# Performance work log

Measured on AMD Instinct MI355X. Metric: run time of the kernel, lower is better.

Reference implementation:

```python
import jax, jax.numpy as jnp
import numpy as np

EMBED = 64
HEADS = 8
N, S = 8, 1024


def setup_inputs() -> dict:
    key = jax.random.key(0)
    ks = jax.random.split(key, 8)
    scale = 1.0 / np.sqrt(EMBED)
    return {
        "values": jax.random.normal(ks[0], (N, S, EMBED), dtype=jnp.float32),
        "keys": jax.random.normal(ks[1], (N, S, EMBED), dtype=jnp.float32),
        "queries": jax.random.normal(ks[2], (N, S, EMBED), dtype=jnp.float32),
        # per-head projection weights, torch Linear convention: y = x @ W.T
        "Wv": jax.random.normal(ks[3], (HEADS, EMBED, EMBED), dtype=jnp.float32) * scale,
        "Wk": jax.random.normal(ks[4], (HEADS, EMBED, EMBED), dtype=jnp.float32) * scale,
        "Wq": jax.random.normal(ks[5], (HEADS, EMBED, EMBED), dtype=jnp.float32) * scale,
        "Wout": jax.random.normal(ks[6], (EMBED, HEADS * EMBED), dtype=jnp.float32) * (1.0 / np.sqrt(HEADS * EMBED)),
        "bout": jnp.zeros((EMBED,), dtype=jnp.float32),
    }


def reference(values, keys, queries, Wv, Wk, Wq, Wout, bout):
    d = queries.shape[-1]
    # Batched per-head projections (each head keeps full embed dim, per the module)
    v = jnp.einsum("nkd,hed->nhke", values, Wv)   # [N,H,K,D]
    k = jnp.einsum("nkd,hed->nhke", keys, Wk)     # [N,H,K,D]
    q = jnp.einsum("nqd,hed->nhqe", queries, Wq)  # [N,H,Q,D]
    energy = jnp.einsum("nhqd,nhkd->nhqk", q, k)
    attn = jax.nn.softmax(energy / jnp.sqrt(jnp.asarray(d, energy.dtype)), axis=-1)  # [N,H,Q,K]
    head_out = jnp.einsum("nhqk,nhkd->nhqd", attn, v)  # [N,H,Q,D]
    # torch.cat(output_heads, dim=2) == transpose heads next to feature then flatten
    nN, nH, nQ, nD = head_out.shape
    cat = jnp.transpose(head_out, (0, 2, 1, 3)).reshape(nN, nQ, nH * nD)  # [N,Q,H*D]
    out = cat @ Wout.T + bout  # [N,Q,D]
    return out, attn
```

## Files before the change

kernel.cpp:

```cpp
#include <hip/hip_runtime.h>

typedef __bf16 bf16x8 __attribute__((ext_vector_type(8)));
typedef float  f32x4  __attribute__((ext_vector_type(4)));

#define MFMA16(a, b, c) __builtin_amdgcn_mfma_f32_16x16x32_bf16((a), (b), (c), 0, 0, 0)

constexpr int N_ = 8, H_ = 8, S_ = 1024, D_ = 64;

__global__ __launch_bounds__(256) void proj_kernel(
    const float* __restrict__ Xq, const float* __restrict__ Xk,
    const float* __restrict__ Xv,
    const float* __restrict__ Wq, const float* __restrict__ Wk,
    const float* __restrict__ Wv,
    unsigned short* __restrict__ qb_, unsigned short* __restrict__ kb_,
    unsigned short* __restrict__ vtb_)
{
    __shared__ __bf16 T[64 * 72];

    const int which = blockIdx.y;
    const float* X = (which == 0) ? Xq : (which == 1) ? Xk : Xv;
    const float* W = (which == 0) ? Wq : (which == 1) ? Wk : Wv;

    const int b   = blockIdx.x;
    const int st  = b & 15;
    const int h   = (b >> 4) & 7;
    const int n   = b >> 7;
    const int s0  = st * 64;
    const int nh  = n * H_ + h;
    const int tid = threadIdx.x;
    const int w = tid >> 6, lane = tid & 63;
    const int l16 = lane & 15, quad = lane >> 4;

    const float* xrow = X + (size_t)(n * S_ + s0 + w * 16 + l16) * D_;
    bf16x8 a[2];
#pragma unroll
    for (int half = 0; half < 2; ++half) {
        const float* p = xrow + half * 32 + quad * 8;
        f32x4 x0 = *(const f32x4*)p;
        f32x4 x1 = *(const f32x4*)(p + 4);
#pragma unroll
        for (int j = 0; j < 4; ++j) { a[half][j] = (__bf16)x0[j]; a[half][4 + j] = (__bf16)x1[j]; }
    }

#pragma unroll
    for (int et = 0; et < 4; ++et) {
        const int e0 = et * 16;
        f32x4 acc = {0.f, 0.f, 0.f, 0.f};
#pragma unroll
        for (int half = 0; half < 2; ++half) {
            const float* wp = W + ((size_t)(h * 64 + e0 + l16)) * 64 + half * 32 + quad * 8;
            f32x4 x0 = *(const f32x4*)wp;
            f32x4 x1 = *(const f32x4*)(wp + 4);
            bf16x8 bf;
#pragma unroll
            for (int j = 0; j < 4; ++j) { bf[j] = (__bf16)x0[j]; bf[4 + j] = (__bf16)x1[j]; }
            acc = MFMA16(a[half], bf, acc);
        }
#pragma unroll
        for (int r = 0; r < 4; ++r) {
            const int sl = w * 16 + quad * 4 + r;
            const int e  = e0 + l16;
            const __bf16 v = (__bf16)acc[r];
            if (which == 2) T[e * 72 + sl] = v;
            else            T[sl * 72 + e] = v;
        }
    }
    __syncthreads();

    const int row = tid >> 2, seg = tid & 3;
    const bf16x8 d0 = *(const bf16x8*)&T[row * 72 + seg * 16];
    const bf16x8 d1 = *(const bf16x8*)&T[row * 72 + seg * 16 + 8];
    __bf16* dst;
    if (which == 2)
        dst = (__bf16*)vtb_ + ((size_t)nh * 64 + row) * S_ + s0 + seg * 16;
    else
        dst = (__bf16*)(which == 0 ? qb_ : kb_) + ((size_t)nh * S_ + s0 + row) * D_ + seg * 16;
    *(bf16x8*)dst = d0;
    *(bf16x8*)(dst + 8) = d1;
}

__global__ __launch_bounds__(256, 4) void attn_kernel(
    const unsigned short* __restrict__ qb_, const unsigned short* __restrict__ kb_,
    const unsigned short* __restrict__ vtb_,
    float* __restrict__ attn_out, unsigned short* __restrict__ catb_)
{
    __shared__ __bf16 P[4 * 2 * 16 * 40];

    const __bf16* qb  = (const __bf16*)qb_;
    const __bf16* kb  = (const __bf16*)kb_;
    const __bf16* vtb = (const __bf16*)vtb_;
    __bf16* catb = (__bf16*)catb_;

    const int b  = blockIdx.x;
    const int qt = b & 15;
    const int h  = (b >> 4) & 7;
    const int n  = b >> 7;
    const int nh = n * H_ + h;
    const int q0 = qt * 64;

    const int tid = threadIdx.x;
    const int w = tid >> 6, lane = tid & 63;
    const int l16 = lane & 15, quad = lane >> 4;
    const int m0 = w * 16;

    const __bf16* qbase = qb + ((size_t)nh * S_ + q0 + m0 + l16) * D_;
    const bf16x8 aq0 = *(const bf16x8*)(qbase + quad * 8);
    const bf16x8 aq1 = *(const bf16x8*)(qbase + 32 + quad * 8);

    const __bf16* kbase = kb + ((size_t)nh * S_ + l16) * D_ + quad * 8;

    f32x4 s4 = {0.f, 0.f, 0.f, 0.f};
#pragma unroll 2
    for (int kt = 0; kt < 64; ++kt) {
        const __bf16* kp = kbase + (size_t)kt * 16 * D_;
        const bf16x8 b0 = *(const bf16x8*)kp;
        const bf16x8 b1 = *(const bf16x8*)(kp + 32);
        f32x4 c = {0.f, 0.f, 0.f, 0.f};
        c = MFMA16(aq0, b0, c);
        c = MFMA16(aq1, b1, c);
#pragma unroll
        for (int r = 0; r < 4; ++r) s4[r] += __expf(c[r] * 0.125f);
    }
#pragma unroll
    for (int off = 1; off < 16; off <<= 1) {
#pragma unroll
        for (int r = 0; r < 4; ++r) s4[r] += __shfl_xor(s4[r], off);
    }
    float inv[4];
#pragma unroll
    for (int r = 0; r < 4; ++r) inv[r] = 1.0f / s4[r];

    float* abase = attn_out + ((size_t)nh * S_ + q0 + m0 + quad * 4) * S_ + l16;
    __bf16* Pw = P + w * (2 * 16 * 40);
    const __bf16* vb = vtb + ((size_t)nh * 64 + l16) * S_ + quad * 8;

    f32x4 acc[4] = {{0.f,0.f,0.f,0.f},{0.f,0.f,0.f,0.f},{0.f,0.f,0.f,0.f},{0.f,0.f,0.f,0.f}};

    for (int ch = 0; ch < 32; ++ch) {
        __bf16* Pt = Pw + (ch & 1) * (16 * 40);
#pragma unroll
        for (int hf = 0; hf < 2; ++hf) {
            const int kt = ch * 2 + hf;
            const __bf16* kp = kbase + (size_t)kt * 16 * D_;
            const bf16x8 b0 = *(const bf16x8*)kp;
            const bf16x8 b1 = *(const bf16x8*)(kp + 32);
            f32x4 c = {0.f, 0.f, 0.f, 0.f};
            c = MFMA16(aq0, b0, c);
            c = MFMA16(aq1, b1, c);
#pragma unroll
            for (int r = 0; r < 4; ++r) {
                const float p = __expf(c[r] * 0.125f) * inv[r];
                abase[(size_t)r * S_ + kt * 16] = p;
                Pt[(quad * 4 + r) * 40 + hf * 16 + l16] = (__bf16)p;
            }
        }
        __builtin_amdgcn_sched_barrier(0);
        __builtin_amdgcn_s_waitcnt(0xC07F);
        const bf16x8 af = *(const bf16x8*)&Pt[l16 * 40 + quad * 8];
        __builtin_amdgcn_sched_barrier(0);
#pragma unroll
        for (int et = 0; et < 4; ++et) {
            const bf16x8 bv = *(const bf16x8*)(vb + (size_t)et * 16 * S_ + ch * 32);
            acc[et] = MFMA16(af, bv, acc[et]);
        }
    }

#pragma unroll
    for (int r = 0; r < 4; ++r) {
        const int s = q0 + m0 + quad * 4 + r;
        __bf16* cp = catb + ((size_t)n * S_ + s) * (H_ * D_) + h * D_ + l16;
#pragma unroll
        for (int et = 0; et < 4; ++et) cp[et * 16] = (__bf16)acc[et][r];
    }
}

__global__ __launch_bounds__(256) void outproj_kernel(
    const unsigned short* __restrict__ catb_, const float* __restrict__ Wout,
    const float* __restrict__ bout, float* __restrict__ out)
{
    __shared__ float R[4 * 16 * 68];

    const __bf16* catb = (const __bf16*)catb_;
    const int r0  = blockIdx.x * 16;
    const int tid = threadIdx.x;
    const int w = tid >> 6, lane = tid & 63;
    const int l16 = lane & 15, quad = lane >> 4;
    const int k0 = w * 128;

    const __bf16* arow  = catb + (size_t)(r0 + l16) * 512 + k0 + quad * 8;
    const float*  wbase = Wout + (size_t)l16 * 512 + k0 + quad * 8;

    f32x4 acc[4] = {{0.f,0.f,0.f,0.f},{0.f,0.f,0.f,0.f},{0.f,0.f,0.f,0.f},{0.f,0.f,0.f,0.f}};

#pragma unroll
    for (int kc = 0; kc < 4; ++kc) {
        const bf16x8 af = *(const bf16x8*)(arow + kc * 32);
#pragma unroll
        for (int et = 0; et < 4; ++et) {
            const float* wp = wbase + (size_t)et * 16 * 512 + kc * 32;
            f32x4 x0 = *(const f32x4*)wp;
            f32x4 x1 = *(const f32x4*)(wp + 4);
            bf16x8 bf;
#pragma unroll
            for (int j = 0; j < 4; ++j) { bf[j] = (__bf16)x0[j]; bf[4 + j] = (__bf16)x1[j]; }
            acc[et] = MFMA16(af, bf, acc[et]);
        }
    }
#pragma unroll
    for (int et = 0; et < 4; ++et)
#pragma unroll
        for (int r = 0; r < 4; ++r)
            R[w * (16 * 68) + (quad * 4 + r) * 68 + et * 16 + l16] = acc[et][r];
    __syncthreads();

    const int row = tid >> 4, c0 = (tid & 15) * 4;
    f32x4 s = *(const f32x4*)&R[row * 68 + c0];
#pragma unroll
    for (int wv = 1; wv < 4; ++wv) s += *(const f32x4*)&R[wv * (16 * 68) + row * 68 + c0];
    s += *(const f32x4*)(bout + c0);
    *(f32x4*)(out + (size_t)(r0 + row) * 64 + c0) = s;
}

extern "C" void kernel_launch(void* const* d_in, const int* in_sizes, int n_in,
                              void* d_out, int out_size, void* d_ws, size_t ws_size,
                              hipStream_t stream)
{
    const float* values  = (const float*)d_in[0];
    const float* keys    = (const float*)d_in[1];
    const float* queries = (const float*)d_in[2];
    const float* Wv      = (const float*)d_in[3];
    const float* Wk      = (const float*)d_in[4];
    const float* Wq      = (const float*)d_in[5];
    const float* Wout    = (const float*)d_in[6];
    const float* bout    = (const float*)d_in[7];

    float* out  = (float*)d_out;
    float* attn = out + (size_t)N_ * S_ * D_;

    const size_t nelem = (size_t)N_ * H_ * S_ * D_;
    unsigned short* qb   = (unsigned short*)d_ws;
    unsigned short* kb   = qb  + nelem;
    unsigned short* vtb  = kb  + nelem;
    unsigned short* catb = vtb + nelem;

    proj_kernel<<<dim3(N_ * H_ * (S_ / 64), 3), 256, 0, stream>>>(
        queries, keys, values, Wq, Wk, Wv, qb, kb, vtb);
    attn_kernel<<<N_ * H_ * (S_ / 64), 256, 0, stream>>>(qb, kb, vtb, attn, catb);
    outproj_kernel<<<(N_ * S_) / 16, 256, 0, stream>>>(catb, Wout, bout, out);
}
```

Measured before the change: 479.8 us.

## Split attention key range across waves with 16-query blocks and LDS reduction

Each attention block now handles 16 queries instead of 64. Its four waves split the 1024 keys into quarters rather than splitting the queries. Softmax row sums and the partial PV outputs are combined across waves through shared memory, and the result is written to catb with vectorized bf16x4 stores. The change also quadruples the grid, raises the occupancy hint, and hoists the V loads ahead of the LDS wait. The goal is more parallelism and more coalesced attn writes, at the cost of extra syncthreads and LDS reduction traffic.

New measurement: 561.1 us. 16.9% more time.

```diff
diff --git a/kernel.cpp b/kernel.cpp
--- a/kernel.cpp
+++ b/kernel.cpp
@@ -1,6 +1,7 @@
 #include <hip/hip_runtime.h>
 
 typedef __bf16 bf16x8 __attribute__((ext_vector_type(8)));
+typedef __bf16 bf16x4 __attribute__((ext_vector_type(4)));
 typedef float  f32x4  __attribute__((ext_vector_type(4)));
 
 #define MFMA16(a, b, c) __builtin_amdgcn_mfma_f32_16x16x32_bf16((a), (b), (c), 0, 0, 0)
@@ -79,12 +80,12 @@
     *(bf16x8*)(dst + 8) = d1;
 }
 
-__global__ __launch_bounds__(256, 4) void attn_kernel(
+__global__ __launch_bounds__(256, 8) void attn_kernel(
     const unsigned short* __restrict__ qb_, const unsigned short* __restrict__ kb_,
     const unsigned short* __restrict__ vtb_,
     float* __restrict__ attn_out, unsigned short* __restrict__ catb_)
 {
-    __shared__ __bf16 P[4 * 2 * 16 * 40];
+    __shared__ float smemF[4 * 16 * 68];
 
     const __bf16* qb  = (const __bf16*)qb_;
     const __bf16* kb  = (const __bf16*)kb_;
@@ -92,26 +93,26 @@
     __bf16* catb = (__bf16*)catb_;
 
     const int b  = blockIdx.x;
-    const int qt = b & 15;
-    const int h  = (b >> 4) & 7;
-    const int n  = b >> 7;
+    const int qt = b & 63;
+    const int h  = (b >> 6) & 7;
+    const int n  = b >> 9;
     const int nh = n * H_ + h;
-    const int q0 = qt * 64;
+    const int q0 = qt * 16;
 
     const int tid = threadIdx.x;
     const int w = tid >> 6, lane = tid & 63;
     const int l16 = lane & 15, quad = lane >> 4;
-    const int m0 = w * 16;
-
-    const __bf16* qbase = qb + ((size_t)nh * S_ + q0 + m0 + l16) * D_;
+    const int k0 = w * 256;
+
+    const __bf16* qbase = qb + ((size_t)nh * S_ + q0 + l16) * D_;
     const bf16x8 aq0 = *(const bf16x8*)(qbase + quad * 8);
     const bf16x8 aq1 = *(const bf16x8*)(qbase + 32 + quad * 8);
 
-    const __bf16* kbase = kb + ((size_t)nh * S_ + l16) * D_ + quad * 8;
+    const __bf16* kbase = kb + ((size_t)(nh * S_ + k0 + l16)) * D_ + quad * 8;
 
     f32x4 s4 = {0.f, 0.f, 0.f, 0.f};
-#pragma unroll 2
-    for (int kt = 0; kt < 64; ++kt) {
+#pragma unroll 4
+    for (int kt = 0; kt < 16; ++kt) {
         const __bf16* kp = kbase + (size_t)kt * 16 * D_;
         const bf16x8 b0 = *(const bf16x8*)kp;
         const bf16x8 b1 = *(const bf16x8*)(kp + 32);
@@ -126,17 +127,25 @@
 #pragma unroll
         for (int r = 0; r < 4; ++r) s4[r] += __shfl_xor(s4[r], off);
     }
+    if (l16 == 0) {
+#pragma unroll
+        for (int r = 0; r < 4; ++r) smemF[w * 16 + quad * 4 + r] = s4[r];
+    }
+    __syncthreads();
     float inv[4];
 #pragma unroll
-    for (int r = 0; r < 4; ++r) inv[r] = 1.0f / s4[r];
-
-    float* abase = attn_out + ((size_t)nh * S_ + q0 + m0 + quad * 4) * S_ + l16;
-    __bf16* Pw = P + w * (2 * 16 * 40);
-    const __bf16* vb = vtb + ((size_t)nh * 64 + l16) * S_ + quad * 8;
+    for (int r = 0; r < 4; ++r) {
+        const int row = quad * 4 + r;
+        inv[r] = 1.0f / (smemF[row] + smemF[16 + row] + smemF[32 + row] + smemF[48 + row]);
+    }
+
+    float* abase = attn_out + ((size_t)(nh * S_ + q0 + quad * 4)) * S_ + k0 + l16;
+    __bf16* Pw = (__bf16*)(smemF + 64) + w * (2 * 16 * 40);
+    const __bf16* vb = vtb + ((size_t)(nh * 64 + l16)) * S_ + k0 + quad * 8;
 
     f32x4 acc[4] = {{0.f,0.f,0.f,0.f},{0.f,0.f,0.f,0.f},{0.f,0.f,0.f,0.f},{0.f,0.f,0.f,0.f}};
 
-    for (int ch = 0; ch < 32; ++ch) {
+    for (int ch = 0; ch < 8; ++ch) {
         __bf16* Pt = Pw + (ch & 1) * (16 * 40);
 #pragma unroll
         for (int hf = 0; hf < 2; ++hf) {
@@ -150,28 +159,38 @@
 #pragma unroll
             for (int r = 0; r < 4; ++r) {
                 const float p = __expf(c[r] * 0.125f) * inv[r];
-                abase[(size_t)r * S_ + kt * 16] = p;
+                abase[(size_t)r * S_ + ch * 32 + hf * 16] = p;
                 Pt[(quad * 4 + r) * 40 + hf * 16 + l16] = (__bf16)p;
             }
         }
+        bf16x8 bv[4];
+#pragma unroll
+        for (int et = 0; et < 4; ++et)
+            bv[et] = *(const bf16x8*)(vb + (size_t)et * 16 * S_ + ch * 32);
         __builtin_amdgcn_sched_barrier(0);
         __builtin_amdgcn_s_waitcnt(0xC07F);
         const bf16x8 af = *(const bf16x8*)&Pt[l16 * 40 + quad * 8];
         __builtin_amdgcn_sched_barrier(0);
 #pragma unroll
-        for (int et = 0; et < 4; ++et) {
-            const bf16x8 bv = *(const bf16x8*)(vb + (size_t)et * 16 * S_ + ch * 32);
-            acc[et] = MFMA16(af, bv, acc[et]);
-        }
-    }
-
-#pragma unroll
-    for (int r = 0; r < 4; ++r) {
-        const int s = q0 + m0 + quad * 4 + r;
-        __bf16* cp = catb + ((size_t)n * S_ + s) * (H_ * D_) + h * D_ + l16;
-#pragma unroll
-        for (int et = 0; et < 4; ++et) cp[et * 16] = (__bf16)acc[et][r];
-    }
+        for (int et = 0; et < 4; ++et) acc[et] = MFMA16(af, bv[et], acc[et]);
+    }
+
+    __syncthreads();
+#pragma unroll
+    for (int et = 0; et < 4; ++et)
+#pragma unroll
+        for (int r = 0; r < 4; ++r)
+            smemF[w * 1088 + (quad * 4 + r) * 68 + et * 16 + l16] = acc[et][r];
+    __syncthreads();
+
+    const int row = tid >> 4, c0 = (tid & 15) * 4;
+    f32x4 s = *(const f32x4*)&smemF[row * 68 + c0];
+#pragma unroll
+    for (int wv = 1; wv < 4; ++wv) s += *(const f32x4*)&smemF[wv * 1088 + row * 68 + c0];
+    bf16x4 o;
+#pragma unroll
+    for (int j = 0; j < 4; ++j) o[j] = (__bf16)s[j];
+    *(bf16x4*)(catb + ((size_t)n * S_ + q0 + row) * (H_ * D_) + h * D_ + c0) = o;
 }
 
 __global__ __launch_bounds__(256) void outproj_kernel(
@@ -245,6 +264,6 @@
 
     proj_kernel<<<dim3(N_ * H_ * (S_ / 64), 3), 256, 0, stream>>>(
         queries, keys, values, Wq, Wk, Wv, qb, kb, vtb);
-    attn_kernel<<<N_ * H_ * (S_ / 64), 256, 0, stream>>>(qb, kb, vtb, attn, catb);
+    attn_kernel<<<N_ * H_ * (S_ / 16), 256, 0, stream>>>(qb, kb, vtb, attn, catb);
     outproj_kernel<<<(N_ * S_) / 16, 256, 0, stream>>>(catb, Wout, bout, out);
 }
```

## Transpose score MFMA layout, shuffle P via bpermute, vectorize attention stores

Applied to the files above, without the earlier changes.

Swaps the MFMA operand order so each lane holds score values for a single query row. This turns the softmax row-sum into a two-step cross-quad shuffle. The LDS staging buffer for the probability tile is replaced by ds_bpermute register shuffles that build the A-operand for the PV MFMA directly. The attention matrix is now written as contiguous float4 pairs per lane instead of scalar strided stores, which targets the large write traffic of the fp32 attn output. In exchange, the stored attn values are now bf16-rounded rather than full fp32, which lowers output precision.

Result: no change. 478.4 us (-0.3%).

```diff
diff --git a/kernel.cpp b/kernel.cpp
--- a/kernel.cpp
+++ b/kernel.cpp
@@ -1,6 +1,7 @@
 #include <hip/hip_runtime.h>
 
 typedef __bf16 bf16x8 __attribute__((ext_vector_type(8)));
+typedef __bf16 bf16x4 __attribute__((ext_vector_type(4)));
 typedef float  f32x4  __attribute__((ext_vector_type(4)));
 
 #define MFMA16(a, b, c) __builtin_amdgcn_mfma_f32_16x16x32_bf16((a), (b), (c), 0, 0, 0)
@@ -84,8 +85,6 @@
     const unsigned short* __restrict__ vtb_,
     float* __restrict__ attn_out, unsigned short* __restrict__ catb_)
 {
-    __shared__ __bf16 P[4 * 2 * 16 * 40];
-
     const __bf16* qb  = (const __bf16*)qb_;
     const __bf16* kb  = (const __bf16*)kb_;
     const __bf16* vtb = (const __bf16*)vtb_;
@@ -103,66 +102,86 @@
     const int l16 = lane & 15, quad = lane >> 4;
     const int m0 = w * 16;
 
-    const __bf16* qbase = qb + ((size_t)nh * S_ + q0 + m0 + l16) * D_;
+    const __bf16* qbase = qb + ((size_t)(nh * S_ + q0 + m0 + l16)) * D_;
     const bf16x8 aq0 = *(const bf16x8*)(qbase + quad * 8);
     const bf16x8 aq1 = *(const bf16x8*)(qbase + 32 + quad * 8);
 
-    const __bf16* kbase = kb + ((size_t)nh * S_ + l16) * D_ + quad * 8;
-
-    f32x4 s4 = {0.f, 0.f, 0.f, 0.f};
-#pragma unroll 2
+    const __bf16* kbase = kb + ((size_t)(nh * S_ + l16)) * D_ + quad * 8;
+
+    float ssum = 0.f;
+#pragma unroll 4
     for (int kt = 0; kt < 64; ++kt) {
         const __bf16* kp = kbase + (size_t)kt * 16 * D_;
         const bf16x8 b0 = *(const bf16x8*)kp;
         const bf16x8 b1 = *(const bf16x8*)(kp + 32);
         f32x4 c = {0.f, 0.f, 0.f, 0.f};
-        c = MFMA16(aq0, b0, c);
-        c = MFMA16(aq1, b1, c);
-#pragma unroll
-        for (int r = 0; r < 4; ++r) s4[r] += __expf(c[r] * 0.125f);
-    }
-#pragma unroll
-    for (int off = 1; off < 16; off <<= 1) {
-#pragma unroll
-        for (int r = 0; r < 4; ++r) s4[r] += __shfl_xor(s4[r], off);
-    }
-    float inv[4];
-#pragma unroll
-    for (int r = 0; r < 4; ++r) inv[r] = 1.0f / s4[r];
-
-    float* abase = attn_out + ((size_t)nh * S_ + q0 + m0 + quad * 4) * S_ + l16;
-    __bf16* Pw = P + w * (2 * 16 * 40);
-    const __bf16* vb = vtb + ((size_t)nh * 64 + l16) * S_ + quad * 8;
+        c = MFMA16(b0, aq0, c);
+        c = MFMA16(b1, aq1, c);
+#pragma unroll
+        for (int r = 0; r < 4; ++r) ssum += __expf(c[r] * 0.125f);
+    }
+    ssum += __shfl_xor(ssum, 16);
+    ssum += __shfl_xor(ssum, 32);
+    const float inv = 1.0f / ssum;
+
+    float* abase = attn_out + ((size_t)(nh * S_ + q0 + m0 + l16)) * S_;
+    const __bf16* vbase = vtb + ((size_t)(nh * 64 + l16)) * S_ + quad * 8;
+
+    const int lo_addr = (((quad & 1) * 2) * 16 + l16) * 4;
+    const int hi_addr = lo_addr + 64;
+    const bool hiq = (quad & 2) != 0;
 
     f32x4 acc[4] = {{0.f,0.f,0.f,0.f},{0.f,0.f,0.f,0.f},{0.f,0.f,0.f,0.f},{0.f,0.f,0.f,0.f}};
 
+#pragma unroll 2
     for (int ch = 0; ch < 32; ++ch) {
-        __bf16* Pt = Pw + (ch & 1) * (16 * 40);
-#pragma unroll
-        for (int hf = 0; hf < 2; ++hf) {
-            const int kt = ch * 2 + hf;
+        unsigned Wt[2][2];
+#pragma unroll
+        for (int t = 0; t < 2; ++t) {
+            const int kt = ch * 2 + t;
             const __bf16* kp = kbase + (size_t)kt * 16 * D_;
             const bf16x8 b0 = *(const bf16x8*)kp;
             const bf16x8 b1 = *(const bf16x8*)(kp + 32);
             f32x4 c = {0.f, 0.f, 0.f, 0.f};
-            c = MFMA16(aq0, b0, c);
-            c = MFMA16(aq1, b1, c);
-#pragma unroll
-            for (int r = 0; r < 4; ++r) {
-                const float p = __expf(c[r] * 0.125f) * inv[r];
-                abase[(size_t)r * S_ + kt * 16] = p;
-                Pt[(quad * 4 + r) * 40 + hf * 16 + l16] = (__bf16)p;
+            c = MFMA16(b0, aq0, c);
+            c = MFMA16(b1, aq1, c);
+            float p[4];
+#pragma unroll
+            for (int r = 0; r < 4; ++r) p[r] = __expf(c[r] * 0.125f) * inv;
+#pragma unroll
+            for (int pr = 0; pr < 2; ++pr) {
+                const __bf16 ha = (__bf16)p[2 * pr], hb = (__bf16)p[2 * pr + 1];
+                const unsigned ua = *(const unsigned short*)&ha;
+                const unsigned ub = *(const unsigned short*)&hb;
+                Wt[t][pr] = ua | (ub << 16);
             }
         }
-        __builtin_amdgcn_sched_barrier(0);
-        __builtin_amdgcn_s_waitcnt(0xC07F);
-        const bf16x8 af = *(const bf16x8*)&Pt[l16 * 40 + quad * 8];
-        __builtin_amdgcn_sched_barrier(0);
+        const int s00 = __builtin_amdgcn_ds_bpermute(lo_addr, (int)Wt[0][0]);
+        const int s10 = __builtin_amdgcn_ds_bpermute(lo_addr, (int)Wt[1][0]);
+        const int s01 = __builtin_amdgcn_ds_bpermute(lo_addr, (int)Wt[0][1]);
+        const int s11 = __builtin_amdgcn_ds_bpermute(lo_addr, (int)Wt[1][1]);
+        const int s02 = __builtin_amdgcn_ds_bpermute(hi_addr, (int)Wt[0][0]);
+        const int s12 = __builtin_amdgcn_ds_bpermute(hi_addr, (int)Wt[1][0]);
+        const int s03 = __builtin_amdgcn_ds_bpermute(hi_addr, (int)Wt[0][1]);
+        const int s13 = __builtin_amdgcn_ds_bpermute(hi_addr, (int)Wt[1][1]);
+        union { bf16x8 v; unsigned u[4]; } pf;
+        pf.u[0] = (unsigned)(hiq ? s10 : s00);
+        pf.u[1] = (unsigned)(hiq ? s11 : s01);
+        pf.u[2] = (unsigned)(hiq ? s12 : s02);
+        pf.u[3] = (unsigned)(hiq ? s13 : s03);
+
 #pragma unroll
         for (int et = 0; et < 4; ++et) {
-            const bf16x8 bv = *(const bf16x8*)(vb + (size_t)et * 16 * S_ + ch * 32);
-            acc[et] = MFMA16(af, bv, acc[et]);
-        }
+            const bf16x8 bv = *(const bf16x8*)(vbase + (size_t)et * 16 * S_ + ch * 32);
+            acc[et] = MFMA16(pf.v, bv, acc[et]);
+        }
+
+        f32x4 f0, f1;
+#pragma unroll
+        for (int j = 0; j < 4; ++j) { f0[j] = (float)pf.v[j]; f1[j] = (float)pf.v[4 + j]; }
+        float* ap = abase + ch * 32 + quad * 8;
+        *(f32x4*)ap = f0;
+        *(f32x4*)(ap + 4) = f1;
     }
 
 #pragma unroll
```
